# Kernel optimization log

Hardware: AMD Instinct MI355X
Metric: run time of the kernel (lower is better)

The kernel has to match this reference:

```python
import jax, jax.numpy as jnp
import numpy as np

B, N, D = 4, 4096, 512
E = 4 * D            # expanded_dim = 2048
TAIL = E // 2        # tail_dim = 1024
HALF = TAIL // 2     # mt_half = 512
HEAD = E - TAIL      # head_dim = 1024
EPS_RMS = 1e-6
EPS_NORM = 1e-12


def setup_inputs() -> dict:
    key = jax.random.key(0)
    k = jax.random.split(key, 6)
    x = jax.random.normal(k[0], (B, N, D), dtype=jnp.float32)
    g = jnp.ones((D,), dtype=jnp.float32)                                   # RMSNorm gain
    W1 = jax.random.normal(k[1], (D, E), dtype=jnp.float32) * 0.02          # Enricher linear
    b1 = jnp.zeros((E,), dtype=jnp.float32)
    V = jax.random.normal(k[2], (N, N), dtype=jnp.float32) * 0.02           # learned positional matrix slice
    bias = jnp.zeros((HALF,), dtype=jnp.float32)                            # contextualizer bias
    Wf = jax.random.normal(k[3], (HEAD + HALF, D), dtype=jnp.float32) * 0.02  # Fuser linear (no bias)
    return {"x": x, "g": g, "W1": W1, "b1": b1, "V": V, "bias": bias, "Wf": Wf}


def reference(x, g, W1, b1, V, bias, Wf):
    # RMSNorm
    xn = x * jax.lax.rsqrt(jnp.mean(jnp.square(x), axis=-1, keepdims=True) + EPS_RMS) * g
    # Enricher: relu(linear)^2
    enriched = jnp.square(jax.nn.relu(xn @ W1 + b1))                        # [B, N, E]
    head = enriched[..., :HEAD]                                             # [B, N, HEAD]
    tail = enriched[..., HEAD:]                                             # [B, N, TAIL]
    # Contextualizer
    x_left = tail[..., :HALF]
    x_right = tail[..., HALF:]
    nrm = jnp.sqrt(jnp.sum(jnp.square(x_right), axis=-1, keepdims=True))
    xr_n = x_right / jnp.maximum(nrm, EPS_NORM)                             # F.normalize, p=2
    cos = jnp.einsum('bnd,bmd->bnm', xr_n, xr_n)                            # [B, N, N] cosine sim
    weighted = V[None, :, :] * cos                                          # elementwise learned V
    ctx = jnp.einsum('bnm,bmd->bnd', weighted, xr_n)                        # chunked-path bmm uses x_right_norm
    ctx = jax.nn.sigmoid(ctx + bias)
    gated = x_left * ctx                                                    # [B, N, HALF]
    # Fuser + residual
    out = jnp.concatenate([head, gated], axis=-1) @ Wf                      # [B, N, D]
    return x + out
```

## Files before the change

kernel.cpp:

```cpp
#include <hip/hip_runtime.h>
#include <stdint.h>

typedef unsigned short u16;
typedef unsigned long long u64;
typedef __attribute__((ext_vector_type(8))) short bf16x8;
typedef __attribute__((ext_vector_type(4))) float f32x4;
typedef __attribute__((ext_vector_type(16))) float f32x16;
typedef __attribute__((ext_vector_type(4))) unsigned int u32x4;
typedef __attribute__((ext_vector_type(4))) unsigned short u16x4;

#define DEV static __device__ __forceinline__

DEV u16 f2bf(float f){
  unsigned u = __builtin_bit_cast(unsigned, f);
  u += 0x7fffu + ((u >> 16) & 1u);
  return (u16)(u >> 16);
}
DEV float bf2f(u16 v){
  unsigned u = ((unsigned)v) << 16;
  return __builtin_bit_cast(float, u);
}

DEV void async_lds16(const void* g, void* l){
  __builtin_amdgcn_global_load_lds(
      (const __attribute__((address_space(1))) unsigned int*)g,
      (__attribute__((address_space(3))) unsigned int*)l, 16, 0, 0);
}

DEV f32x4 mfma16(bf16x8 a, bf16x8 b, f32x4 c){
  return __builtin_amdgcn_mfma_f32_16x16x32_bf16(a, b, c, 0, 0, 0);
}
DEV f32x16 mfma32(bf16x8 a, bf16x8 b, f32x16 c){
  return __builtin_amdgcn_mfma_f32_32x32x16_bf16(a, b, c, 0, 0, 0);
}

__global__ __launch_bounds__(64) void k_rms(const float* __restrict__ x,
                                            const float* __restrict__ g,
                                            u16* __restrict__ xn){
  const int row = blockIdx.x;
  const int l = threadIdx.x;
  const float* xr = x + (size_t)row * 512 + l * 8;
  f32x4 a = *(const f32x4*)xr;
  f32x4 c = *(const f32x4*)(xr + 4);
  float s = a[0]*a[0]+a[1]*a[1]+a[2]*a[2]+a[3]*a[3]
          + c[0]*c[0]+c[1]*c[1]+c[2]*c[2]+c[3]*c[3];
  #pragma unroll
  for (int off = 32; off >= 1; off >>= 1) s += __shfl_xor(s, off);
  float sc = rsqrtf(s * (1.f/512.f) + 1e-6f);
  f32x4 g0 = *(const f32x4*)&g[l*8];
  f32x4 g1 = *(const f32x4*)&g[l*8+4];
  u32x4 o;
  o[0] = (unsigned)f2bf(a[0]*sc*g0[0]) | ((unsigned)f2bf(a[1]*sc*g0[1]) << 16);
  o[1] = (unsigned)f2bf(a[2]*sc*g0[2]) | ((unsigned)f2bf(a[3]*sc*g0[3]) << 16);
  o[2] = (unsigned)f2bf(c[0]*sc*g1[0]) | ((unsigned)f2bf(c[1]*sc*g1[1]) << 16);
  o[3] = (unsigned)f2bf(c[2]*sc*g1[2]) | ((unsigned)f2bf(c[3]*sc*g1[3]) << 16);
  *(u32x4*)&xn[(size_t)row*512 + l*8] = o;
}

__global__ __launch_bounds__(64) void k_norm(const float* __restrict__ xr_in,
                                             u16* __restrict__ xrn){
  const int row = blockIdx.x;
  const int l = threadIdx.x;
  const float* xr = xr_in + (size_t)row * 512 + l * 8;
  f32x4 a = *(const f32x4*)xr;
  f32x4 c = *(const f32x4*)(xr + 4);
  float s = a[0]*a[0]+a[1]*a[1]+a[2]*a[2]+a[3]*a[3]
          + c[0]*c[0]+c[1]*c[1]+c[2]*c[2]+c[3]*c[3];
  #pragma unroll
  for (int off = 32; off >= 1; off >>= 1) s += __shfl_xor(s, off);
  float sc = 1.f / fmaxf(sqrtf(s), 1e-12f);
  u32x4 o;
  o[0] = (unsigned)f2bf(a[0]*sc) | ((unsigned)f2bf(a[1]*sc) << 16);
  o[1] = (unsigned)f2bf(a[2]*sc) | ((unsigned)f2bf(a[3]*sc) << 16);
  o[2] = (unsigned)f2bf(c[0]*sc) | ((unsigned)f2bf(c[1]*sc) << 16);
  o[3] = (unsigned)f2bf(c[2]*sc) | ((unsigned)f2bf(c[3]*sc) << 16);
  *(u32x4*)&xrn[(size_t)row*512 + l*8] = o;
}

__global__ __launch_bounds__(256) void k_tr32(const float* __restrict__ in,
                                              u16* __restrict__ out, int R, int C){
  __shared__ float tile[32][33];
  const int t = threadIdx.x;
  const int r = t >> 3;
  const int c4 = (t & 7) << 2;
  const int r0 = blockIdx.y << 5, c0 = blockIdx.x << 5;
  f32x4 v = *(const f32x4*)&in[(size_t)(r0 + r) * C + c0 + c4];
  tile[r][c4+0]=v[0]; tile[r][c4+1]=v[1]; tile[r][c4+2]=v[2]; tile[r][c4+3]=v[3];
  __syncthreads();
  u64 o =
      (u64)f2bf(tile[c4+0][r])
    | ((u64)f2bf(tile[c4+1][r]) << 16)
    | ((u64)f2bf(tile[c4+2][r]) << 32)
    | ((u64)f2bf(tile[c4+3][r]) << 48);
  *(u64*)&out[(size_t)(c0 + r) * R + r0 + c4] = o;
}

__global__ __launch_bounds__(256) void k_trb(const u16* __restrict__ in,
                                             u16* __restrict__ out, int R, int C){
  __shared__ u16 tile[32][40];
  const int t = threadIdx.x;
  const int r = t >> 3;
  const int c4 = (t & 7) << 2;
  const size_t bb = (size_t)blockIdx.z * R * C;
  const int r0 = blockIdx.y << 5, c0 = blockIdx.x << 5;
  u64 v = *(const u64*)&in[bb + (size_t)(r0 + r)*C + c0 + c4];
  tile[r][c4+0]=(u16)v; tile[r][c4+1]=(u16)(v>>16);
  tile[r][c4+2]=(u16)(v>>32); tile[r][c4+3]=(u16)(v>>48);
  __syncthreads();
  u64 o =
      (u64)tile[c4+0][r]
    | ((u64)tile[c4+1][r] << 16)
    | ((u64)tile[c4+2][r] << 32)
    | ((u64)tile[c4+3][r] << 48);
  *(u64*)&out[bb + (size_t)(c0 + r) * R + r0 + c4] = o;
}

__global__ __launch_bounds__(256) void k_gemm1(const u16* __restrict__ A,
                                               const u16* __restrict__ Bt,
                                               const float* __restrict__ b1,
                                               u16* __restrict__ head,
                                               float* __restrict__ xleft,
                                               float* __restrict__ xright){
  __shared__ u16 As[128*32];
  __shared__ u16 Bs[128*32];
  const int t = threadIdx.x;
  const int l = t & 63;
  const int w = t >> 6;
  const int wr = w >> 1, wc = w & 1;
  const int m0 = blockIdx.x << 7;
  const int n0 = blockIdx.y << 7;
  const int ra = t >> 2;
  const int kb = (t & 3) << 3;
  const int lr = l & 15, lh = l >> 4;
  f32x4 acc[4][4];
  #pragma unroll
  for (int i=0;i<4;i++)
    #pragma unroll
    for (int j=0;j<4;j++)
      #pragma unroll
      for (int r=0;r<4;r++) acc[i][j][r] = 0.f;
  for (int k0 = 0; k0 < 512; k0 += 32){
    async_lds16(A  + (size_t)(m0 + ra)*512      + k0 + kb, &As[t*8]);
    async_lds16(A  + (size_t)(m0 + 64 + ra)*512 + k0 + kb, &As[2048 + t*8]);
    async_lds16(Bt + (size_t)(n0 + ra)*512      + k0 + kb, &Bs[t*8]);
    async_lds16(Bt + (size_t)(n0 + 64 + ra)*512 + k0 + kb, &Bs[2048 + t*8]);
    __syncthreads();
    bf16x8 af[4], bfr[4];
    #pragma unroll
    for (int i=0;i<4;i++){
      af[i]  = *(const bf16x8*)&As[(wr*64 + i*16 + lr)*32 + lh*8];
      bfr[i] = *(const bf16x8*)&Bs[(wc*64 + i*16 + lr)*32 + lh*8];
    }
    #pragma unroll
    for (int i=0;i<4;i++)
      #pragma unroll
      for (int j=0;j<4;j++)
        acc[i][j] = mfma16(af[i], bfr[j], acc[i][j]);
    __syncthreads();
  }
  #pragma unroll
  for (int i=0;i<4;i++){
    #pragma unroll
    for (int j=0;j<4;j++){
      int c = n0 + wc*64 + j*16 + lr;
      float bb = b1[c];
      #pragma unroll
      for (int r=0;r<4;r++){
        int m = m0 + wr*64 + i*16 + lh*4 + r;
        float v = acc[i][j][r] + bb;
        v = v > 0.f ? v*v : 0.f;
        if (c < 1024)      head[(size_t)m*1024 + c] = f2bf(v);
        else if (c < 1536) xleft[(size_t)m*512 + (c - 1024)] = v;
        else               xright[(size_t)m*512 + (c - 1536)] = v;
      }
    }
  }
}

__global__ __launch_bounds__(256) void k_gemm3(const u16* __restrict__ head,
                                               const u16* __restrict__ gated,
                                               const u16* __restrict__ Wft,
                                               const float* __restrict__ x,
                                               float* __restrict__ out){
  __shared__ u16 As[128*32];
  __shared__ u16 Bs[128*32];
  const int t = threadIdx.x;
  const int l = t & 63;
  const int w = t >> 6;
  const int wr = w >> 1, wc = w & 1;
  const int m0 = blockIdx.x << 7;
  const int n0 = blockIdx.y << 7;
  const int ra = t >> 2;
  const int kb = (t & 3) << 3;
  const int lr = l & 15, lh = l >> 4;
  f32x4 acc[4][4];
  #pragma unroll
  for (int i=0;i<4;i++)
    #pragma unroll
    for (int j=0;j<4;j++)
      #pragma unroll
      for (int r=0;r<4;r++) acc[i][j][r] = 0.f;
  for (int k0 = 0; k0 < 1536; k0 += 32){
    const u16* sa; size_t lda; int kk;
    if (k0 < 1024){ sa = head;  lda = 1024; kk = k0; }
    else          { sa = gated; lda = 512;  kk = k0 - 1024; }
    async_lds16(sa + (size_t)(m0 + ra)*lda      + kk + kb, &As[t*8]);
    async_lds16(sa + (size_t)(m0 + 64 + ra)*lda + kk + kb, &As[2048 + t*8]);
    async_lds16(Wft + (size_t)(n0 + ra)*1536      + k0 + kb, &Bs[t*8]);
    async_lds16(Wft + (size_t)(n0 + 64 + ra)*1536 + k0 + kb, &Bs[2048 + t*8]);
    __syncthreads();
    bf16x8 af[4], bfr[4];
    #pragma unroll
    for (int i=0;i<4;i++){
      af[i]  = *(const bf16x8*)&As[(wr*64 + i*16 + lr)*32 + lh*8];
      bfr[i] = *(const bf16x8*)&Bs[(wc*64 + i*16 + lr)*32 + lh*8];
    }
    #pragma unroll
    for (int i=0;i<4;i++)
      #pragma unroll
      for (int j=0;j<4;j++)
        acc[i][j] = mfma16(af[i], bfr[j], acc[i][j]);
    __syncthreads();
  }
  #pragma unroll
  for (int i=0;i<4;i++){
    #pragma unroll
    for (int j=0;j<4;j++){
      int c = n0 + wc*64 + j*16 + lr;
      #pragma unroll
      for (int r=0;r<4;r++){
        int m = m0 + wr*64 + i*16 + lh*4 + r;
        size_t gi = (size_t)m*512 + c;
        out[gi] = x[gi] + acc[i][j][r];
      }
    }
  }
}

__global__ __launch_bounds__(512, 2) void k_attn(const u16* __restrict__ xrn,
                                                 const u16* __restrict__ xrT,
                                                 const float* __restrict__ V,
                                                 const float* __restrict__ bias,
                                                 const float* __restrict__ xleft,
                                                 u16* __restrict__ gated){
  __shared__ char smem[154624];
  char* km = smem;
  char* tq = smem + 65536;
  char* ps = smem + 131072;
  char* pb = smem + 149504;
  const int t = threadIdx.x;
  const int l = t & 63, w = t >> 6;
  const int wr = w >> 2, ks = w & 3, wc = (w >> 1) & 1, kq2 = w & 1;
  const int lo = l & 31, hi = l >> 5;
  const int bid = blockIdx.x;
  const int b  = (bid & 7) >> 1;
  const int n0 = ((((bid >> 3) << 1) | (bid & 1))) << 6;
  const u16* xb  = xrn + (size_t)b * (4096*512);
  const u16* xTb = xrT + (size_t)b * (512*4096);

  bf16x8 areg[8];
  {
    const u16* apt = xb + (size_t)(n0 + wr*32 + lo)*512 + ks*128 + hi*8;
    #pragma unroll
    for (int kq = 0; kq < 8; ++kq) areg[kq] = *(const bf16x8*)(apt + kq*16);
  }
  f32x16 acc[8];
  #pragma unroll
  for (int i = 0; i < 8; ++i)
    #pragma unroll
    for (int j = 0; j < 16; ++j) acc[i][j] = 0.f;

  const int prf = t >> 3;
  const int pc4 = (t & 7) << 2;
  const int wrr = prf >> 5, prr = prf & 31;

  #pragma unroll
  for (int c = 0; c < 4; ++c){
    int off = (c*512 + t)*16;
    int row = off >> 10, colb = off & 1023;
    async_lds16(xb + (size_t)row*512 + ((colb ^ ((row&15)<<4)) >> 1), km + off);
    int r   = off >> 8;
    int lg  = (off & 255) ^ ((r & 15) << 4);
    int q   = lg >> 6;
    int mc  = (lg & 63) >> 1;
    async_lds16(xTb + (size_t)(q*128 + r)*4096 + mc, tq + off);
  }
  __syncthreads();

  int cur = 0;
  for (int it = 0; it < 128; ++it){
    const int m0 = it << 5;
    f32x4 vf = *(const f32x4*)&V[(size_t)(n0 + prf)*4096 + m0 + pc4];
    if (it < 127){
      const int m1 = m0 + 32;
      const int nb = (cur ^ 1) * 32768;
      #pragma unroll
      for (int c = 0; c < 4; ++c){
        int off = (c*512 + t)*16;
        int row = off >> 10, colb = off & 1023;
        async_lds16(xb + (size_t)(m1 + row)*512 + ((colb ^ ((row&15)<<4)) >> 1),
                    km + nb + off);
        int r   = off >> 8;
        int lg  = (off & 255) ^ ((r & 15) << 4);
        int q   = lg >> 6;
        int mc  = (lg & 63) >> 1;
        async_lds16(xTb + (size_t)(q*128 + r)*4096 + m1 + mc, tq + nb + off);
      }
    }
    f32x16 S0, S1;
    #pragma unroll
    for (int j = 0; j < 16; ++j){ S0[j] = 0.f; S1[j] = 0.f; }
    {
      const char* kbp = km + cur*32768 + lo*1024;
      const int swk = (lo & 15) << 4;
      #pragma unroll
      for (int kq = 0; kq < 8; kq += 2){
        bf16x8 b0 = *(const bf16x8*)(kbp + ((ks*256 + kq*32 + hi*16) ^ swk));
        bf16x8 b1 = *(const bf16x8*)(kbp + ((ks*256 + (kq+1)*32 + hi*16) ^ swk));
        S0 = mfma32(areg[kq],   b0, S0);
        S1 = mfma32(areg[kq+1], b1, S1);
      }
    }
    {
      char* pw = ps + ((wr*4 + ks)*32)*72 + lo*2;
      #pragma unroll
      for (int rg = 0; rg < 16; ++rg){
        int prow = (rg & 3) + 8*(rg >> 2) + 4*hi;
        *(u16*)(pw + prow*72) = f2bf(S0[rg] + S1[rg]);
      }
    }
    asm volatile("s_waitcnt lgkmcnt(0)" ::: "memory");
    __builtin_amdgcn_s_barrier();
    __builtin_amdgcn_sched_barrier(0);
    {
      float s0=0.f, s1=0.f, s2=0.f, s3=0.f;
      #pragma unroll
      for (int k2 = 0; k2 < 4; ++k2){
        u16x4 pv = *(const u16x4*)(ps + (((wrr*4 + k2)*32 + prr)*36 + pc4)*2);
        s0 += bf2f(pv[0]); s1 += bf2f(pv[1]); s2 += bf2f(pv[2]); s3 += bf2f(pv[3]);
      }
      u64 po = (u64)f2bf(s0 * vf[0])
             | ((u64)f2bf(s1 * vf[1]) << 16)
             | ((u64)f2bf(s2 * vf[2]) << 32)
             | ((u64)f2bf(s3 * vf[3]) << 48);
      *(u64*)(pb + prf*72 + pc4*2) = po;
    }
    asm volatile("s_waitcnt lgkmcnt(0)" ::: "memory");
    __builtin_amdgcn_s_barrier();
    __builtin_amdgcn_sched_barrier(0);
    {
      bf16x8 pa = *(const bf16x8*)(pb + (wr*32 + lo)*72 + kq2*32 + hi*16);
      const char* tb = tq + cur*32768;
      #pragma unroll
      for (int ds = 0; ds < 8; ++ds){
        int d = wc*256 + ds*32 + lo;
        int r = d & 127, q = d >> 7;
        bf16x8 bfr = *(const bf16x8*)(tb + r*256 +
                       ((q*64 + kq2*32 + hi*16) ^ ((r & 15) << 4)));
        acc[ds] = mfma32(pa, bfr, acc[ds]);
      }
    }
    __syncthreads();
    cur ^= 1;
  }

  float* red = (float*)smem;
  const int rbase = (wr*2 + wc) * 8192;
  if (kq2 == 1){
    #pragma unroll
    for (int ds = 0; ds < 8; ++ds)
      #pragma unroll
      for (int rg = 0; rg < 16; ++rg)
        red[rbase + (ds*16 + rg)*64 + l] = acc[ds][rg];
  }
  __syncthreads();
  if (kq2 == 0){
    #pragma unroll
    for (int ds = 0; ds < 8; ++ds){
      const int d = wc*256 + ds*32 + lo;
      const float bs = bias[d];
      #pragma unroll
      for (int rg = 0; rg < 16; ++rg){
        int row = n0 + wr*32 + (rg & 3) + 8*(rg >> 2) + 4*hi;
        float v = acc[ds][rg] + red[rbase + (ds*16 + rg)*64 + l] + bs;
        v = 1.f / (1.f + __expf(-v));
        size_t gi = (size_t)(b*4096 + row)*512 + d;
        gated[gi] = f2bf(xleft[gi] * v);
      }
    }
  }
}

extern "C" void kernel_launch(void* const* d_in, const int* in_sizes, int n_in,
                              void* d_out, int out_size, void* d_ws, size_t ws_size,
                              hipStream_t stream){
  const float* x    = (const float*)d_in[0];
  const float* g    = (const float*)d_in[1];
  const float* W1   = (const float*)d_in[2];
  const float* b1   = (const float*)d_in[3];
  const float* V    = (const float*)d_in[4];
  const float* bias = (const float*)d_in[5];
  const float* Wf   = (const float*)d_in[6];
  float* out = (float*)d_out;

  char* ws = (char*)d_ws;
  const size_t MB = 1024u*1024u;
  u16*   xn     = (u16*)  (ws + 0*MB);
  u16*   W1t    = (u16*)  (ws + 16*MB);
  u16*   Wft    = (u16*)  (ws + 18*MB);
  u16*   head   = (u16*)  (ws + 20*MB);
  float* xleft  = (float*)(ws + 52*MB);
  float* xright = (float*)(ws + 84*MB);
  u16*   gated  = (u16*)  (ws + 84*MB);
  u16*   xrn    = (u16*)  (ws + 116*MB);
  u16*   xrT    = (u16*)  (ws + 132*MB);

  k_rms  <<<dim3(16384),      dim3(64),  0, stream>>>(x, g, xn);
  k_tr32 <<<dim3(64, 16),     dim3(256), 0, stream>>>(W1, W1t, 512, 2048);
  k_tr32 <<<dim3(16, 48),     dim3(256), 0, stream>>>(Wf, Wft, 1536, 512);
  k_gemm1<<<dim3(128, 16),    dim3(256), 0, stream>>>(xn, W1t, b1, head, xleft, xright);
  k_norm <<<dim3(16384),      dim3(64),  0, stream>>>(xright, xrn);
  k_trb  <<<dim3(16, 128, 4), dim3(256), 0, stream>>>(xrn, xrT, 4096, 512);
  k_attn <<<dim3(256),        dim3(512), 0, stream>>>(xrn, xrT, V, bias, xleft, gated);
  k_gemm3<<<dim3(128, 4),     dim3(256), 0, stream>>>(head, gated, Wft, x, out);
}
```

Baseline: 404.0 us.

## Double-buffer GEMM LDS tiles and re-layout attention LDS swizzles

Both dense GEMM kernels now keep two LDS buffers for the A and B tiles and issue the next k-slice's async loads before computing on the current one. This removes one barrier per iteration and lets global-load latency overlap the MFMA work, at the cost of doubling LDS use per block. In the attention kernel, the transposed xr tile is stored row-per-feature with a new XOR swizzle, the K-tile swizzle is narrowed to 8 rows, and the P buffer row stride changes from 72 to 80 bytes. These layout changes aim to reduce LDS bank conflicts.

```diff
diff --git a/kernel.cpp b/kernel.cpp
--- a/kernel.cpp
+++ b/kernel.cpp
@@ -121,8 +121,8 @@
                                                u16* __restrict__ head,
                                                float* __restrict__ xleft,
                                                float* __restrict__ xright){
-  __shared__ u16 As[128*32];
-  __shared__ u16 Bs[128*32];
+  __shared__ u16 As[2][128*32];
+  __shared__ u16 Bs[2][128*32];
   const int t = threadIdx.x;
   const int l = t & 63;
   const int w = t >> 6;
@@ -139,17 +139,28 @@
     for (int j=0;j<4;j++)
       #pragma unroll
       for (int r=0;r<4;r++) acc[i][j][r] = 0.f;
+
+  async_lds16(A  + (size_t)(m0 + ra)*512      + kb, &As[0][t*8]);
+  async_lds16(A  + (size_t)(m0 + 64 + ra)*512 + kb, &As[0][2048 + t*8]);
+  async_lds16(Bt + (size_t)(n0 + ra)*512      + kb, &Bs[0][t*8]);
+  async_lds16(Bt + (size_t)(n0 + 64 + ra)*512 + kb, &Bs[0][2048 + t*8]);
+  __syncthreads();
+
+  int cur = 0;
   for (int k0 = 0; k0 < 512; k0 += 32){
-    async_lds16(A  + (size_t)(m0 + ra)*512      + k0 + kb, &As[t*8]);
-    async_lds16(A  + (size_t)(m0 + 64 + ra)*512 + k0 + kb, &As[2048 + t*8]);
-    async_lds16(Bt + (size_t)(n0 + ra)*512      + k0 + kb, &Bs[t*8]);
-    async_lds16(Bt + (size_t)(n0 + 64 + ra)*512 + k0 + kb, &Bs[2048 + t*8]);
-    __syncthreads();
+    if (k0 + 32 < 512){
+      const int kn = k0 + 32;
+      const int nb = cur ^ 1;
+      async_lds16(A  + (size_t)(m0 + ra)*512      + kn + kb, &As[nb][t*8]);
+      async_lds16(A  + (size_t)(m0 + 64 + ra)*512 + kn + kb, &As[nb][2048 + t*8]);
+      async_lds16(Bt + (size_t)(n0 + ra)*512      + kn + kb, &Bs[nb][t*8]);
+      async_lds16(Bt + (size_t)(n0 + 64 + ra)*512 + kn + kb, &Bs[nb][2048 + t*8]);
+    }
     bf16x8 af[4], bfr[4];
     #pragma unroll
     for (int i=0;i<4;i++){
-      af[i]  = *(const bf16x8*)&As[(wr*64 + i*16 + lr)*32 + lh*8];
-      bfr[i] = *(const bf16x8*)&Bs[(wc*64 + i*16 + lr)*32 + lh*8];
+      af[i]  = *(const bf16x8*)&As[cur][(wr*64 + i*16 + lr)*32 + lh*8];
+      bfr[i] = *(const bf16x8*)&Bs[cur][(wc*64 + i*16 + lr)*32 + lh*8];
     }
     #pragma unroll
     for (int i=0;i<4;i++)
@@ -157,6 +168,7 @@
       for (int j=0;j<4;j++)
         acc[i][j] = mfma16(af[i], bfr[j], acc[i][j]);
     __syncthreads();
+    cur ^= 1;
   }
   #pragma unroll
   for (int i=0;i<4;i++){
@@ -182,8 +194,8 @@
                                                const u16* __restrict__ Wft,
                                                const float* __restrict__ x,
                                                float* __restrict__ out){
-  __shared__ u16 As[128*32];
-  __shared__ u16 Bs[128*32];
+  __shared__ u16 As[2][128*32];
+  __shared__ u16 Bs[2][128*32];
   const int t = threadIdx.x;
   const int l = t & 63;
   const int w = t >> 6;
@@ -200,20 +212,27 @@
     for (int j=0;j<4;j++)
       #pragma unroll
       for (int r=0;r<4;r++) acc[i][j][r] = 0.f;
-  for (int k0 = 0; k0 < 1536; k0 += 32){
+
+  auto stage = [&](int nb, int k0){
     const u16* sa; size_t lda; int kk;
     if (k0 < 1024){ sa = head;  lda = 1024; kk = k0; }
     else          { sa = gated; lda = 512;  kk = k0 - 1024; }
-    async_lds16(sa + (size_t)(m0 + ra)*lda      + kk + kb, &As[t*8]);
-    async_lds16(sa + (size_t)(m0 + 64 + ra)*lda + kk + kb, &As[2048 + t*8]);
-    async_lds16(Wft + (size_t)(n0 + ra)*1536      + k0 + kb, &Bs[t*8]);
-    async_lds16(Wft + (size_t)(n0 + 64 + ra)*1536 + k0 + kb, &Bs[2048 + t*8]);
-    __syncthreads();
+    async_lds16(sa + (size_t)(m0 + ra)*lda      + kk + kb, &As[nb][t*8]);
+    async_lds16(sa + (size_t)(m0 + 64 + ra)*lda + kk + kb, &As[nb][2048 + t*8]);
+    async_lds16(Wft + (size_t)(n0 + ra)*1536      + k0 + kb, &Bs[nb][t*8]);
+    async_lds16(Wft + (size_t)(n0 + 64 + ra)*1536 + k0 + kb, &Bs[nb][2048 + t*8]);
+  };
+  stage(0, 0);
+  __syncthreads();
+
+  int cur = 0;
+  for (int k0 = 0; k0 < 1536; k0 += 32){
+    if (k0 + 32 < 1536) stage(cur ^ 1, k0 + 32);
     bf16x8 af[4], bfr[4];
     #pragma unroll
     for (int i=0;i<4;i++){
-      af[i]  = *(const bf16x8*)&As[(wr*64 + i*16 + lr)*32 + lh*8];
-      bfr[i] = *(const bf16x8*)&Bs[(wc*64 + i*16 + lr)*32 + lh*8];
+      af[i]  = *(const bf16x8*)&As[cur][(wr*64 + i*16 + lr)*32 + lh*8];
+      bfr[i] = *(const bf16x8*)&Bs[cur][(wc*64 + i*16 + lr)*32 + lh*8];
     }
     #pragma unroll
     for (int i=0;i<4;i++)
@@ -221,6 +240,7 @@
       for (int j=0;j<4;j++)
         acc[i][j] = mfma16(af[i], bfr[j], acc[i][j]);
     __syncthreads();
+    cur ^= 1;
   }
   #pragma unroll
   for (int i=0;i<4;i++){
@@ -245,7 +265,7 @@
                                                  u16* __restrict__ gated){
   __shared__ char smem[154624];
   char* km = smem;
-  char* tq = smem + 65536;
+  char* tt = smem + 65536;
   char* ps = smem + 131072;
   char* pb = smem + 149504;
   const int t = threadIdx.x;
@@ -278,12 +298,9 @@
   for (int c = 0; c < 4; ++c){
     int off = (c*512 + t)*16;
     int row = off >> 10, colb = off & 1023;
-    async_lds16(xb + (size_t)row*512 + ((colb ^ ((row&15)<<4)) >> 1), km + off);
-    int r   = off >> 8;
-    int lg  = (off & 255) ^ ((r & 15) << 4);
-    int q   = lg >> 6;
-    int mc  = (lg & 63) >> 1;
-    async_lds16(xTb + (size_t)(q*128 + r)*4096 + mc, tq + off);
+    async_lds16(xb + (size_t)row*512 + ((colb ^ ((row&7)<<4)) >> 1), km + off);
+    int dr = off >> 6, cb2 = off & 63;
+    async_lds16(xTb + (size_t)dr*4096 + ((cb2 ^ ((dr&6)<<3)) >> 1), tt + off);
   }
   __syncthreads();
 
@@ -298,13 +315,11 @@
       for (int c = 0; c < 4; ++c){
         int off = (c*512 + t)*16;
         int row = off >> 10, colb = off & 1023;
-        async_lds16(xb + (size_t)(m1 + row)*512 + ((colb ^ ((row&15)<<4)) >> 1),
+        async_lds16(xb + (size_t)(m1 + row)*512 + ((colb ^ ((row&7)<<4)) >> 1),
                     km + nb + off);
-        int r   = off >> 8;
-        int lg  = (off & 255) ^ ((r & 15) << 4);
-        int q   = lg >> 6;
-        int mc  = (lg & 63) >> 1;
-        async_lds16(xTb + (size_t)(q*128 + r)*4096 + m1 + mc, tq + nb + off);
+        int dr = off >> 6, cb2 = off & 63;
+        async_lds16(xTb + (size_t)dr*4096 + m1 + ((cb2 ^ ((dr&6)<<3)) >> 1),
+                    tt + nb + off);
       }
     }
     f32x16 S0, S1;
@@ -312,7 +327,7 @@
     for (int j = 0; j < 16; ++j){ S0[j] = 0.f; S1[j] = 0.f; }
     {
       const char* kbp = km + cur*32768 + lo*1024;
-      const int swk = (lo & 15) << 4;
+      const int swk = (lo & 7) << 4;
       #pragma unroll
       for (int kq = 0; kq < 8; kq += 2){
         bf16x8 b0 = *(const bf16x8*)(kbp + ((ks*256 + kq*32 + hi*16) ^ swk));
@@ -343,20 +358,19 @@
              | ((u64)f2bf(s1 * vf[1]) << 16)
              | ((u64)f2bf(s2 * vf[2]) << 32)
              | ((u64)f2bf(s3 * vf[3]) << 48);
-      *(u64*)(pb + prf*72 + pc4*2) = po;
+      *(u64*)(pb + (prf*40 + pc4)*2) = po;
     }
     asm volatile("s_waitcnt lgkmcnt(0)" ::: "memory");
     __builtin_amdgcn_s_barrier();
     __builtin_amdgcn_sched_barrier(0);
     {
-      bf16x8 pa = *(const bf16x8*)(pb + (wr*32 + lo)*72 + kq2*32 + hi*16);
-      const char* tb = tq + cur*32768;
+      bf16x8 pa = *(const bf16x8*)(pb + (wr*32 + lo)*80 + kq2*32 + hi*16);
+      const char* tb = tt + cur*32768;
       #pragma unroll
       for (int ds = 0; ds < 8; ++ds){
-        int d = wc*256 + ds*32 + lo;
-        int r = d & 127, q = d >> 7;
-        bf16x8 bfr = *(const bf16x8*)(tb + r*256 +
-                       ((q*64 + kq2*32 + hi*16) ^ ((r & 15) << 4)));
+        int drow = wc*256 + ds*32 + lo;
+        bf16x8 bfr = *(const bf16x8*)(tb + drow*64 +
+                       ((kq2*32 + hi*16) ^ ((drow & 6) << 3)));
         acc[ds] = mfma32(pa, bfr, acc[ds]);
       }
     }
```

Measured after the change: 385.0 us. -4.7%, faster.
